# Kernel optimization log

Measured on AMD Instinct MI355X. Metric: run time of the kernel, lower is better.

The kernel has to match this reference:

```python
import jax, jax.numpy as jnp
import numpy as np

N = 50000
E = 800000
H = 8
DH = 32  # hidden 256 / heads 8


def gat_layer(h, src, dst, W, a_src, a_dst, b):
    # h: [N, 256] -> per-head projected features [N, H, DH]
    hp = (h @ W).reshape(N, H, DH)
    # per-node attention logits for src/dst roles: [N, H]
    s_src = jnp.einsum('nhd,hd->nh', hp, a_src)
    s_dst = jnp.einsum('nhd,hd->nh', hp, a_dst)
    e = jax.nn.leaky_relu(s_src[src] + s_dst[dst], negative_slope=0.2)  # [Et, H]
    # segment softmax over incoming edges of each dst node
    m = jax.ops.segment_max(e, dst, num_segments=N)  # [N, H]
    ex = jnp.exp(e - m[dst])
    denom = jax.ops.segment_sum(ex, dst, num_segments=N)  # [N, H] (>0: self-loops)
    alpha = ex / denom[dst]  # [Et, H]
    out = jax.ops.segment_sum(alpha[:, :, None] * hp[src], dst, num_segments=N)
    return out.reshape(N, H * DH) + b


def han_forward(x, edges, proj_W, proj_b, gat_W, gat_asrc, gat_adst, gat_b,
                sem_W1, sem_b1, sem_W2, cls_W1, cls_b1, cls_W2, cls_b2):
    h0 = x @ proj_W + proj_b  # [N, 256]
    loop = jnp.arange(N, dtype=edges.dtype)
    embs = []
    for p in range(edges.shape[0]):  # 3 meta-paths (fixed, small)
        src = jnp.concatenate([edges[p, 0], loop])  # add self-loops (PyG default)
        dst = jnp.concatenate([edges[p, 1], loop])
        h = h0
        for l in range(2):  # 2 GAT layers per meta-path
            h = gat_layer(h, src, dst, gat_W[p, l], gat_asrc[p, l], gat_adst[p, l], gat_b[p, l])
            h = jax.nn.elu(h)  # dropout: eval-mode no-op
        embs.append(h)
    emb = jnp.stack(embs, axis=1)  # [N, P, 256]
    scores = (jnp.tanh(emb @ sem_W1 + sem_b1) @ sem_W2).squeeze(-1)  # [N, P]
    w = jax.nn.softmax(scores, axis=1)
    z = jnp.sum(emb * w[:, :, None], axis=1)  # [N, 256]
    hcls = jax.nn.relu(z @ cls_W1 + cls_b1)
    logits = hcls @ cls_W2 + cls_b2  # [N, 2]
    return logits


def setup_inputs() -> dict:
    key = jax.random.key(0)
    ks = jax.random.split(key, 16)
    s = 0.05
    return {
        'x': jax.random.normal(ks[0], (N, 128), jnp.float32),
        'edges': jax.random.randint(ks[1], (3, 2, E), 0, N, dtype=jnp.int32),
        'proj_W': jax.random.normal(ks[2], (128, 256), jnp.float32) * s,
        'proj_b': jnp.zeros((256,), jnp.float32),
        'gat_W': jax.random.normal(ks[3], (3, 2, 256, 256), jnp.float32) * s,
        'gat_asrc': jax.random.normal(ks[4], (3, 2, H, DH), jnp.float32) * s,
        'gat_adst': jax.random.normal(ks[5], (3, 2, H, DH), jnp.float32) * s,
        'gat_b': jnp.zeros((3, 2, 256), jnp.float32),
        'sem_W1': jax.random.normal(ks[6], (256, 128), jnp.float32) * s,
        'sem_b1': jnp.zeros((128,), jnp.float32),
        'sem_W2': jax.random.normal(ks[7], (128, 1), jnp.float32) * s,
        'cls_W1': jax.random.normal(ks[8], (256, 128), jnp.float32) * s,
        'cls_b1': jnp.zeros((128,), jnp.float32),
        'cls_W2': jax.random.normal(ks[9], (128, 2), jnp.float32) * s,
        'cls_b2': jnp.zeros((2,), jnp.float32),
    }


def reference(x, edges, proj_W, proj_b, gat_W, gat_asrc, gat_adst, gat_b,
              sem_W1, sem_b1, sem_W2, cls_W1, cls_b1, cls_W2, cls_b2):
    return han_forward(x, edges, proj_W, proj_b, gat_W, gat_asrc, gat_adst, gat_b,
                       sem_W1, sem_b1, sem_W2, cls_W1, cls_b1, cls_W2, cls_b2)
```

## Files before the change

kernel.cpp:

```cpp
#include <hip/hip_runtime.h>
#include <hip/hip_fp16.h>
#include <math.h>

#define N_NODES 50000
#define N_EDG   800000
#define NH      8
#define DH      32
#define HID     256
#define MAXD    64

typedef __attribute__((ext_vector_type(8))) short bf16x8;
typedef __attribute__((ext_vector_type(4))) float f32x4;

__device__ __forceinline__ unsigned short f2bf(float x) {
    unsigned u = __float_as_uint(x);
    u += 0x7FFF + ((u >> 16) & 1);
    return (unsigned short)(u >> 16);
}
__device__ __forceinline__ float bf2f(unsigned short h) {
    return __uint_as_float(((unsigned)h) << 16);
}
__device__ __forceinline__ void split8(const float4& a, const float4& b,
                                       uint4& hi, uint4& lo) {
    float v[8] = {a.x,a.y,a.z,a.w,b.x,b.y,b.z,b.w};
    unsigned short h[8], l[8];
    #pragma unroll
    for (int i = 0; i < 8; ++i) { h[i] = f2bf(v[i]); l[i] = f2bf(v[i] - bf2f(h[i])); }
    hi = make_uint4(h[0]|((unsigned)h[1]<<16), h[2]|((unsigned)h[3]<<16),
                    h[4]|((unsigned)h[5]<<16), h[6]|((unsigned)h[7]<<16));
    lo = make_uint4(l[0]|((unsigned)l[1]<<16), l[2]|((unsigned)l[3]<<16),
                    l[4]|((unsigned)l[5]<<16), l[6]|((unsigned)l[7]<<16));
}
__device__ __forceinline__ void h8_to_pair(uint4 r, uint4& hi, uint4& lo) {
    const __half2* hp = (const __half2*)&r;
    unsigned short h[8], l[8];
    #pragma unroll
    for (int i = 0; i < 4; ++i) {
        float2 f = __half22float2(hp[i]);
        h[2*i]   = f2bf(f.x); l[2*i]   = f2bf(f.x - bf2f(h[2*i]));
        h[2*i+1] = f2bf(f.y); l[2*i+1] = f2bf(f.y - bf2f(h[2*i+1]));
    }
    hi = make_uint4(h[0]|((unsigned)h[1]<<16), h[2]|((unsigned)h[3]<<16),
                    h[4]|((unsigned)h[5]<<16), h[6]|((unsigned)h[7]<<16));
    lo = make_uint4(l[0]|((unsigned)l[1]<<16), l[2]|((unsigned)l[3]<<16),
                    l[4]|((unsigned)l[5]<<16), l[6]|((unsigned)l[7]<<16));
}
__device__ __forceinline__ void gll16(const unsigned short* g, unsigned short* l) {
    __builtin_amdgcn_global_load_lds(
        (const __attribute__((address_space(1))) void*)g,
        (__attribute__((address_space(3))) void*)l, 16, 0, 0);
}

template<int NC, int ACT, int OUTMODE, int AMODE>
__global__ __launch_bounds__(256)
void mfma_gemm_k(const float* __restrict__ A32p, const __half* __restrict__ A16p,
                 int lda,
                 const unsigned short* __restrict__ WThi,
                 const unsigned short* __restrict__ WTlo,
                 const float* __restrict__ bias,
                 float* __restrict__ C, __half* __restrict__ Ch,
                 int ldc, int M, int K) {
    __shared__ unsigned short sAh[128*32], sAl[128*32], sBh[128*32], sBl[128*32];
    const int tid  = threadIdx.x;
    const int lane = tid & 63;
    const int w    = tid >> 6;
    const int wr   = w >> 1, wc = w & 1;
    const int r0   = blockIdx.x * 128;
    const int c0   = blockIdx.y * 128;
    const int l15  = lane & 15, q = lane >> 4;

    const int cl8   = (((lane & 3) ^ ((lane >> 4) & 3)) << 3);
    const int lrow  = w*32 + (lane >> 2);
    const int gbrow0 = c0 + lrow, gbrow1 = c0 + lrow + 16;
    const int lbase = w * 1024;

    const int srow = tid >> 2, slot = tid & 3;
    const size_t ga0 = (size_t)min(r0 + srow,      M - 1) * lda + slot * 8;
    const size_t ga1 = (size_t)min(r0 + srow + 64, M - 1) * lda + slot * 8;
    const int lda0 = srow*32 + ((slot ^ ((srow >> 2) & 3)) << 3);
    const int lda1 = lda0 + 64*32;

    f32x4 acc[4][4];
    #pragma unroll
    for (int i = 0; i < 4; ++i)
        #pragma unroll
        for (int j = 0; j < 4; ++j) acc[i][j] = (f32x4){0.f, 0.f, 0.f, 0.f};

    const int swzF = (l15 >> 2) & 3;
    const int qs   = ((q ^ swzF) << 3);

    const int nsteps = K >> 5;
    for (int s = 0; s < nsteps; ++s) {
        const int kc = s << 5;
        __syncthreads();
        uint4 h0, l0, h1, l1;
        if constexpr (AMODE == 0) {
            float4 f0a = *(const float4*)&A32p[ga0 + kc];
            float4 f0b = *(const float4*)&A32p[ga0 + kc + 4];
            float4 f1a = *(const float4*)&A32p[ga1 + kc];
            float4 f1b = *(const float4*)&A32p[ga1 + kc + 4];
            split8(f0a, f0b, h0, l0);
            split8(f1a, f1b, h1, l1);
        } else {
            uint4 r0v = *(const uint4*)&A16p[ga0 + kc];
            uint4 r1v = *(const uint4*)&A16p[ga1 + kc];
            h8_to_pair(r0v, h0, l0);
            h8_to_pair(r1v, h1, l1);
        }
        *(uint4*)&sAh[lda0] = h0; *(uint4*)&sAl[lda0] = l0;
        *(uint4*)&sAh[lda1] = h1; *(uint4*)&sAl[lda1] = l1;
        gll16(&WThi[(size_t)gbrow0*K + kc + cl8], &sBh[lbase]);
        gll16(&WThi[(size_t)gbrow1*K + kc + cl8], &sBh[lbase + 512]);
        gll16(&WTlo[(size_t)gbrow0*K + kc + cl8], &sBl[lbase]);
        gll16(&WTlo[(size_t)gbrow1*K + kc + cl8], &sBl[lbase + 512]);
        __syncthreads();

        bf16x8 fAh[4], fAl[4];
        #pragma unroll
        for (int t = 0; t < 4; ++t) {
            int ra = (wr*64 + t*16 + l15) * 32 + qs;
            fAh[t] = *(const bf16x8*)&sAh[ra];
            fAl[t] = *(const bf16x8*)&sAl[ra];
        }
        #pragma unroll
        for (int nt = 0; nt < 4; ++nt) {
            int rb = (wc*64 + nt*16 + l15) * 32 + qs;
            bf16x8 fBh = *(const bf16x8*)&sBh[rb];
            bf16x8 fBl = *(const bf16x8*)&sBl[rb];
            #pragma unroll
            for (int mt = 0; mt < 4; ++mt) {
                acc[mt][nt] = __builtin_amdgcn_mfma_f32_16x16x32_bf16(fAh[mt], fBh, acc[mt][nt], 0, 0, 0);
                acc[mt][nt] = __builtin_amdgcn_mfma_f32_16x16x32_bf16(fAh[mt], fBl, acc[mt][nt], 0, 0, 0);
                acc[mt][nt] = __builtin_amdgcn_mfma_f32_16x16x32_bf16(fAl[mt], fBh, acc[mt][nt], 0, 0, 0);
            }
        }
    }
    #pragma unroll
    for (int mt = 0; mt < 4; ++mt)
        #pragma unroll
        for (int nt = 0; nt < 4; ++nt) {
            int col = c0 + wc*64 + nt*16 + l15;
            float bb = bias ? bias[col] : 0.f;
            #pragma unroll
            for (int r = 0; r < 4; ++r) {
                int grow = r0 + wr*64 + mt*16 + q*4 + r;
                if (grow < M) {
                    float v = acc[mt][nt][r] + bb;
                    if (ACT == 1) v = tanhf(v);
                    else if (ACT == 2) v = fmaxf(v, 0.f);
                    size_t o = (size_t)grow * ldc + col;
                    if (OUTMODE == 2) Ch[o] = __float2half(v);
                    else              C[o] = v;
                }
            }
        }
}

__global__ __launch_bounds__(256)
void mfma_gemm3_k(const __half* __restrict__ A16p, int aoffz, int lda,
                  const unsigned short* __restrict__ WT, int l,
                  __half* __restrict__ hp3, int M) {
    __shared__ unsigned short sAh[128*32], sAl[128*32], sBh[128*32], sBl[128*32];
    const int p = blockIdx.z;
    A16p += (size_t)p * aoffz;
    const unsigned short* WThi = WT + (size_t)(2*p + l) * 131072;
    const unsigned short* WTlo = WThi + 65536;
    __half* Ch = hp3 + (size_t)p * N_NODES * HID;
    const int K = HID;

    const int tid  = threadIdx.x;
    const int lane = tid & 63;
    const int w    = tid >> 6;
    const int wr   = w >> 1, wc = w & 1;
    const int r0   = blockIdx.x * 128;
    const int c0   = blockIdx.y * 128;
    const int l15  = lane & 15, q = lane >> 4;

    const int cl8   = (((lane & 3) ^ ((lane >> 4) & 3)) << 3);
    const int lrow  = w*32 + (lane >> 2);
    const int gbrow0 = c0 + lrow, gbrow1 = c0 + lrow + 16;
    const int lbase = w * 1024;

    const int srow = tid >> 2, slot = tid & 3;
    const size_t ga0 = (size_t)min(r0 + srow,      M - 1) * lda + slot * 8;
    const size_t ga1 = (size_t)min(r0 + srow + 64, M - 1) * lda + slot * 8;
    const int lda0 = srow*32 + ((slot ^ ((srow >> 2) & 3)) << 3);
    const int lda1 = lda0 + 64*32;

    f32x4 acc[4][4];
    #pragma unroll
    for (int i = 0; i < 4; ++i)
        #pragma unroll
        for (int j = 0; j < 4; ++j) acc[i][j] = (f32x4){0.f, 0.f, 0.f, 0.f};

    const int swzF = (l15 >> 2) & 3;
    const int qs   = ((q ^ swzF) << 3);

    for (int s = 0; s < 8; ++s) {
        const int kc = s << 5;
        __syncthreads();
        uint4 r0v = *(const uint4*)&A16p[ga0 + kc];
        uint4 r1v = *(const uint4*)&A16p[ga1 + kc];
        uint4 h0, l0, h1, l1;
        h8_to_pair(r0v, h0, l0);
        h8_to_pair(r1v, h1, l1);
        *(uint4*)&sAh[lda0] = h0; *(uint4*)&sAl[lda0] = l0;
        *(uint4*)&sAh[lda1] = h1; *(uint4*)&sAl[lda1] = l1;
        gll16(&WThi[(size_t)gbrow0*K + kc + cl8], &sBh[lbase]);
        gll16(&WThi[(size_t)gbrow1*K + kc + cl8], &sBh[lbase + 512]);
        gll16(&WTlo[(size_t)gbrow0*K + kc + cl8], &sBl[lbase]);
        gll16(&WTlo[(size_t)gbrow1*K + kc + cl8], &sBl[lbase + 512]);
        __syncthreads();

        bf16x8 fAh[4], fAl[4];
        #pragma unroll
        for (int t = 0; t < 4; ++t) {
            int ra = (wr*64 + t*16 + l15) * 32 + qs;
            fAh[t] = *(const bf16x8*)&sAh[ra];
            fAl[t] = *(const bf16x8*)&sAl[ra];
        }
        #pragma unroll
        for (int nt = 0; nt < 4; ++nt) {
            int rb = (wc*64 + nt*16 + l15) * 32 + qs;
            bf16x8 fBh = *(const bf16x8*)&sBh[rb];
            bf16x8 fBl = *(const bf16x8*)&sBl[rb];
            #pragma unroll
            for (int mt = 0; mt < 4; ++mt) {
                acc[mt][nt] = __builtin_amdgcn_mfma_f32_16x16x32_bf16(fAh[mt], fBh, acc[mt][nt], 0, 0, 0);
                acc[mt][nt] = __builtin_amdgcn_mfma_f32_16x16x32_bf16(fAh[mt], fBl, acc[mt][nt], 0, 0, 0);
                acc[mt][nt] = __builtin_amdgcn_mfma_f32_16x16x32_bf16(fAl[mt], fBh, acc[mt][nt], 0, 0, 0);
            }
        }
    }
    #pragma unroll
    for (int mt = 0; mt < 4; ++mt)
        #pragma unroll
        for (int nt = 0; nt < 4; ++nt) {
            int col = c0 + wc*64 + nt*16 + l15;
            #pragma unroll
            for (int r = 0; r < 4; ++r) {
                int grow = r0 + wr*64 + mt*16 + q*4 + r;
                if (grow < M)
                    Ch[(size_t)grow * HID + col] = __float2half(acc[mt][nt][r]);
            }
        }
}

__global__ __launch_bounds__(256)
void cvtWall_k(const float* __restrict__ gatW, const float* __restrict__ projW,
               const float* __restrict__ semW1, const float* __restrict__ clsW1,
               unsigned short* __restrict__ WT) {
    int y = blockIdx.y;
    const float* W; int K, N;
    if (y < 6)       { W = gatW + (size_t)y * 65536; K = 256; N = 256; }
    else if (y == 6) { W = projW; K = 128; N = 256; }
    else if (y == 7) { W = semW1; K = 256; N = 128; }
    else             { W = clsW1; K = 256; N = 128; }
    int idx = blockIdx.x * 256 + threadIdx.x;
    if (idx >= K * N) return;
    unsigned short* hi = WT + (size_t)y * 131072;
    unsigned short* lo = hi + 65536;
    int k = idx / N, n = idx - k * N;
    float v = W[idx];
    unsigned short h = f2bf(v);
    hi[n * K + k] = h;
    lo[n * K + k] = f2bf(v - bf2f(h));
}

__global__ __launch_bounds__(256)
void attn_scores3_k(const __half* __restrict__ hp3,
                    const float* __restrict__ gatAs, const float* __restrict__ gatAd,
                    int l, float* __restrict__ ssrc3, float* __restrict__ sdst3) {
    int p = blockIdx.y;
    int gid = blockIdx.x * 256 + threadIdx.x;
    if (gid >= N_NODES * NH) return;
    int h = gid & 7;
    const __half2* hv = (const __half2*)(hp3 + (size_t)p * N_NODES * HID + (size_t)gid * DH);
    const float* a = gatAs + (2*p + l) * HID + h * DH;
    const float* d = gatAd + (2*p + l) * HID + h * DH;
    float ss = 0.f, sd = 0.f;
    #pragma unroll
    for (int j = 0; j < 8; ++j) {
        float4 av = ((const float4*)a)[j], dv = ((const float4*)d)[j];
        float2 f0 = __half22float2(hv[2*j]);
        float2 f1 = __half22float2(hv[2*j + 1]);
        ss += f0.x*av.x + f0.y*av.y + f1.x*av.z + f1.y*av.w;
        sd += f0.x*dv.x + f0.y*dv.y + f1.x*dv.z + f1.y*dv.w;
    }
    ssrc3[p * N_NODES * NH + gid] = ss;
    sdst3[p * N_NODES * NH + gid] = sd;
}

__global__ __launch_bounds__(256)
void zero_k(int* p, int n) { int i = blockIdx.x*256 + threadIdx.x; if (i < n) p[i] = 0; }

__global__ __launch_bounds__(256)
void fill1_k(const int* __restrict__ edges, int* __restrict__ cnt3,
             unsigned short* __restrict__ slots3) {
    int e = blockIdx.x*256 + threadIdx.x;
    if (e >= 3*N_EDG) return;
    int p = e / N_EDG, i = e - p * N_EDG;
    const int* src = edges + (size_t)p * 2 * N_EDG;
    const int* dst = src + N_EDG;
    int s = src[i], d = dst[i];
    s = min(max(s, 0), N_NODES - 1);
    d = min(max(d, 0), N_NODES - 1);
    int pos = atomicAdd(&cnt3[p * N_NODES + d], 1);
    if (pos < MAXD)
        slots3[((size_t)p * N_NODES + d) * MAXD + pos] = (unsigned short)s;
}

__global__ __launch_bounds__(256)
void agg3_k(const int* __restrict__ cnt3, const unsigned short* __restrict__ slots3,
            const float* __restrict__ ssrc3, const float* __restrict__ sdst3,
            const __half* __restrict__ hp3, const float* __restrict__ gatB, int l,
            __half* __restrict__ emb16) {
    const int p = blockIdx.y;
    int wid  = (blockIdx.x * blockDim.x + threadIdx.x) >> 6;
    int lane = threadIdx.x & 63;
    if (wid >= N_NODES) return;
    const int n = wid;
    const unsigned short* srcs = slots3 + ((size_t)p * N_NODES + n) * MAXD;
    const float* s_src = ssrc3 + p * N_NODES * NH;
    const float* s_dst = sdst3 + p * N_NODES * NH;
    const __half* hp = hp3 + (size_t)p * N_NODES * HID;
    const float* bias = gatB + (2*p + l) * HID;
    const int deg = min(cnt3[p * N_NODES + n], MAXD);

    const int sub = lane & 31, eo = lane >> 5;
    const int h2  = sub >> 2;
    const float sd2 = s_dst[n*NH + h2];
    float dn = 0.f;
    float a0=0.f,a1=0.f,a2=0.f,a3=0.f,a4=0.f,a5=0.f,a6=0.f,a7=0.f;
    for (int i = eo; i < deg; i += 2) {
        int s = srcs[i];
        float ev = s_src[s*NH + h2] + sd2;
        ev = ev > 0.f ? ev : 0.2f * ev;
        float ww = __expf(ev);
        dn += ww;
        const __half2* hv = (const __half2*)(hp + (size_t)s * HID + sub * 8);
        __half2 p0 = hv[0], p1 = hv[1], p2 = hv[2], p3 = hv[3];
        float2 f0 = __half22float2(p0), f1 = __half22float2(p1);
        float2 f2 = __half22float2(p2), f3 = __half22float2(p3);
        a0 += ww*f0.x; a1 += ww*f0.y; a2 += ww*f1.x; a3 += ww*f1.y;
        a4 += ww*f2.x; a5 += ww*f2.y; a6 += ww*f3.x; a7 += ww*f3.y;
    }
    dn += __shfl_xor(dn, 32);
    a0 += __shfl_xor(a0, 32); a1 += __shfl_xor(a1, 32);
    a2 += __shfl_xor(a2, 32); a3 += __shfl_xor(a3, 32);
    a4 += __shfl_xor(a4, 32); a5 += __shfl_xor(a5, 32);
    a6 += __shfl_xor(a6, 32); a7 += __shfl_xor(a7, 32);
    if (lane < 32) {
        float evs = s_src[n*NH + h2] + sd2;
        evs = evs > 0.f ? evs : 0.2f * evs;
        float ws = __expf(evs);
        dn += ws;
        const __half2* hv = (const __half2*)(hp + (size_t)n * HID + sub * 8);
        float2 f0 = __half22float2(hv[0]), f1 = __half22float2(hv[1]);
        float2 f2 = __half22float2(hv[2]), f3 = __half22float2(hv[3]);
        a0 += ws*f0.x; a1 += ws*f0.y; a2 += ws*f1.x; a3 += ws*f1.y;
        a4 += ws*f2.x; a5 += ws*f2.y; a6 += ws*f3.x; a7 += ws*f3.y;

        float rdn = 1.f / dn;
        float v[8] = {a0,a1,a2,a3,a4,a5,a6,a7};
        const float4 b0 = *(const float4*)&bias[sub*8];
        const float4 b1 = *(const float4*)&bias[sub*8 + 4];
        v[0]=v[0]*rdn+b0.x; v[1]=v[1]*rdn+b0.y; v[2]=v[2]*rdn+b0.z; v[3]=v[3]*rdn+b0.w;
        v[4]=v[4]*rdn+b1.x; v[5]=v[5]*rdn+b1.y; v[6]=v[6]*rdn+b1.z; v[7]=v[7]*rdn+b1.w;
        unsigned short hh[8];
        #pragma unroll
        for (int k = 0; k < 8; ++k) {
            float e = v[k] > 0.f ? v[k] : expm1f(v[k]);
            hh[k] = __half_as_ushort(__float2half(e));
        }
        size_t o = (size_t)n * 768 + p * HID + sub * 8;
        *(uint4*)&emb16[o] = make_uint4(hh[0]|((unsigned)hh[1]<<16), hh[2]|((unsigned)hh[3]<<16),
                                        hh[4]|((unsigned)hh[5]<<16), hh[6]|((unsigned)hh[7]<<16));
    }
}

__global__ __launch_bounds__(256)
void score_z_k(const float* t, const float* __restrict__ W2,
               const __half* __restrict__ emb16, float* z) {
    int wid  = (blockIdx.x * blockDim.x + threadIdx.x) >> 6;
    int lane = threadIdx.x & 63;
    if (wid >= N_NODES) return;
    const int n = wid;
    float sc[3];
    #pragma unroll
    for (int p = 0; p < 3; ++p) {
        const float* tr = t + (size_t)(n*3 + p) * 128;
        float part = tr[lane] * W2[lane] + tr[64 + lane] * W2[64 + lane];
        #pragma unroll
        for (int o = 1; o < 64; o <<= 1) part += __shfl_xor(part, o);
        sc[p] = part;
    }
    float m  = fmaxf(sc[0], fmaxf(sc[1], sc[2]));
    float e0 = __expf(sc[0]-m), e1 = __expf(sc[1]-m), e2 = __expf(sc[2]-m);
    float rs = 1.f / (e0 + e1 + e2);
    e0 *= rs; e1 *= rs; e2 *= rs;
    const __half* er = emb16 + (size_t)n * 768;
    for (int c = lane; c < 256; c += 64) {
        float v0 = __half2float(er[c]);
        float v1 = __half2float(er[256 + c]);
        float v2 = __half2float(er[512 + c]);
        z[(size_t)n*384 + c] = e0*v0 + e1*v1 + e2*v2;
    }
}

__global__ __launch_bounds__(256)
void logits_k(const float* __restrict__ hcls, const float* __restrict__ W2,
              const float* __restrict__ b2, float* __restrict__ out) {
    int gid = blockIdx.x*256 + threadIdx.x;
    if (gid >= N_NODES * 2) return;
    int n = gid >> 1, o = gid & 1;
    const float* hr = hcls + (size_t)n * 128;
    float a = b2[o];
    #pragma unroll 4
    for (int j = 0; j < 128; ++j) a += hr[j] * W2[j*2 + o];
    out[gid] = a;
}

extern "C" void kernel_launch(void* const* d_in, const int* in_sizes, int n_in,
                              void* d_out, int out_size, void* d_ws, size_t ws_size,
                              hipStream_t stream) {
    (void)in_sizes; (void)n_in; (void)out_size; (void)ws_size;
    const float* x     = (const float*)d_in[0];
    const int*   edges = (const int*)  d_in[1];
    const float* projW = (const float*)d_in[2];
    const float* projb = (const float*)d_in[3];
    const float* gatW  = (const float*)d_in[4];
    const float* gatAs = (const float*)d_in[5];
    const float* gatAd = (const float*)d_in[6];
    const float* gatB  = (const float*)d_in[7];
    const float* semW1 = (const float*)d_in[8];
    const float* semb1 = (const float*)d_in[9];
    const float* semW2 = (const float*)d_in[10];
    const float* clsW1 = (const float*)d_in[11];
    const float* clsb1 = (const float*)d_in[12];
    const float* clsW2 = (const float*)d_in[13];
    const float* clsb2 = (const float*)d_in[14];
    float* out = (float*)d_out;

    char* base = (char*)d_ws;
    const size_t PLANE = (size_t)N_NODES * HID * 2;
    __half* hp3   = (__half*)(base);
    __half* emb16 = (__half*)(base + 3*PLANE);
    __half* h016  = (__half*)(base + 6*PLANE);
    char* small = base + 7*PLANE;
    float* ssrc3 = (float*)small;
    float* sdst3 = ssrc3 + 3*(size_t)N_NODES*NH;
    int*   cnt3  = (int*)(sdst3 + 3*(size_t)N_NODES*NH);
    unsigned short* WT = (unsigned short*)(cnt3 + 3*N_NODES);
    unsigned short* slots3 = WT + 9*131072;
    float* tbuf = (float*)base;
    float* hcls = (float*)(base + 6*PLANE);

    dim3 blk(256);
    const int gx = (N_NODES + 127) / 128;

    cvtWall_k<<<dim3(256, 9), blk, 0, stream>>>(gatW, projW, semW1, clsW1, WT);
    zero_k  <<<(3*N_NODES+255)/256, blk, 0, stream>>>(cnt3, 3*N_NODES);
    fill1_k <<<(3*N_EDG+255)/256,   blk, 0, stream>>>(edges, cnt3, slots3);

    mfma_gemm_k<256,0,2,0><<<dim3(gx,2), blk, 0, stream>>>(
        x, nullptr, 128, WT + 6*131072, WT + 6*131072 + 65536, projb,
        nullptr, h016, 256, N_NODES, 128);

    for (int l = 0; l < 2; ++l) {
        if (l == 0)
            mfma_gemm3_k<<<dim3(gx,2,3), blk, 0, stream>>>(
                h016, 0, HID, WT, 0, hp3, N_NODES);
        else
            mfma_gemm3_k<<<dim3(gx,2,3), blk, 0, stream>>>(
                emb16, HID, 3*HID, WT, 1, hp3, N_NODES);
        attn_scores3_k<<<dim3((N_NODES*NH+255)/256, 3), blk, 0, stream>>>(
            hp3, gatAs, gatAd, l, ssrc3, sdst3);
        agg3_k<<<dim3((N_NODES*64)/256, 3), blk, 0, stream>>>(
            cnt3, slots3, ssrc3, sdst3, hp3, gatB, l, emb16);
    }

    mfma_gemm_k<128,1,0,1><<<dim3((150000+127)/128, 1), blk, 0, stream>>>(
        nullptr, emb16, 256, WT + 7*131072, WT + 7*131072 + 65536, semb1,
        tbuf, nullptr, 128, 150000, 256);
    score_z_k<<<(N_NODES*64)/256, blk, 0, stream>>>(tbuf, semW2, emb16, tbuf);
    mfma_gemm_k<128,2,0,0><<<dim3(gx, 1), blk, 0, stream>>>(
        tbuf, nullptr, 384, WT + 8*131072, WT + 8*131072 + 65536, clsb1,
        hcls, nullptr, 128, N_NODES, 256);
    logits_k<<<(N_NODES*2+255)/256, blk, 0, stream>>>(hcls, clsW2, clsb2, out);
}
```

Before: 1.062 ms.

## Switch split-precision GEMMs from bf16 to scaled fp16 and drop A lo-split

Replaces the bf16 hi/lo split emulation of fp32 GEMMs with an fp16 hi plus scaled fp16 lo split. The lo part is multiplied by 2048 to avoid underflow and accumulated separately. Because the A operand is already fp16, the gemm3 and AMODE 1 paths now load it directly into LDS with global_load_lds. That removes the per-element conversion and split work and one of the three MFMAs per tile. The risks are lower accuracy for the dropped A-lo term and fp16 range limits, plus more registers from the second accumulator set.

After: 1.116 ms. 1.05x slower.

```diff
diff --git a/kernel.cpp b/kernel.cpp
--- a/kernel.cpp
+++ b/kernel.cpp
@@ -8,44 +8,28 @@
 #define DH      32
 #define HID     256
 #define MAXD    64
-
-typedef __attribute__((ext_vector_type(8))) short bf16x8;
+#define LOSC    2048.0f
+#define RLOSC   4.8828125e-4f
+
+typedef __attribute__((ext_vector_type(8))) _Float16 f16x8;
 typedef __attribute__((ext_vector_type(4))) float f32x4;
 
-__device__ __forceinline__ unsigned short f2bf(float x) {
-    unsigned u = __float_as_uint(x);
-    u += 0x7FFF + ((u >> 16) & 1);
-    return (unsigned short)(u >> 16);
-}
-__device__ __forceinline__ float bf2f(unsigned short h) {
-    return __uint_as_float(((unsigned)h) << 16);
-}
-__device__ __forceinline__ void split8(const float4& a, const float4& b,
-                                       uint4& hi, uint4& lo) {
+__device__ __forceinline__ void splitH8(const float4& a, const float4& b,
+                                        uint4& hi, uint4& lo) {
     float v[8] = {a.x,a.y,a.z,a.w,b.x,b.y,b.z,b.w};
     unsigned short h[8], l[8];
     #pragma unroll
-    for (int i = 0; i < 8; ++i) { h[i] = f2bf(v[i]); l[i] = f2bf(v[i] - bf2f(h[i])); }
+    for (int i = 0; i < 8; ++i) {
+        __half hh = __float2half(v[i]);
+        h[i] = __half_as_ushort(hh);
+        l[i] = __half_as_ushort(__float2half((v[i] - __half2float(hh)) * LOSC));
+    }
     hi = make_uint4(h[0]|((unsigned)h[1]<<16), h[2]|((unsigned)h[3]<<16),
                     h[4]|((unsigned)h[5]<<16), h[6]|((unsigned)h[7]<<16));
     lo = make_uint4(l[0]|((unsigned)l[1]<<16), l[2]|((unsigned)l[3]<<16),
                     l[4]|((unsigned)l[5]<<16), l[6]|((unsigned)l[7]<<16));
 }
-__device__ __forceinline__ void h8_to_pair(uint4 r, uint4& hi, uint4& lo) {
-    const __half2* hp = (const __half2*)&r;
-    unsigned short h[8], l[8];
-    #pragma unroll
-    for (int i = 0; i < 4; ++i) {
-        float2 f = __half22float2(hp[i]);
-        h[2*i]   = f2bf(f.x); l[2*i]   = f2bf(f.x - bf2f(h[2*i]));
-        h[2*i+1] = f2bf(f.y); l[2*i+1] = f2bf(f.y - bf2f(h[2*i+1]));
-    }
-    hi = make_uint4(h[0]|((unsigned)h[1]<<16), h[2]|((unsigned)h[3]<<16),
-                    h[4]|((unsigned)h[5]<<16), h[6]|((unsigned)h[7]<<16));
-    lo = make_uint4(l[0]|((unsigned)l[1]<<16), l[2]|((unsigned)l[3]<<16),
-                    l[4]|((unsigned)l[5]<<16), l[6]|((unsigned)l[7]<<16));
-}
-__device__ __forceinline__ void gll16(const unsigned short* g, unsigned short* l) {
+__device__ __forceinline__ void gll16(const void* g, void* l) {
     __builtin_amdgcn_global_load_lds(
         (const __attribute__((address_space(1))) void*)g,
         (__attribute__((address_space(3))) void*)l, 16, 0, 0);
@@ -71,6 +55,8 @@
 
     const int cl8   = (((lane & 3) ^ ((lane >> 4) & 3)) << 3);
     const int lrow  = w*32 + (lane >> 2);
+    const int garow0 = min(r0 + lrow,      M - 1);
+    const int garow1 = min(r0 + lrow + 16, M - 1);
     const int gbrow0 = c0 + lrow, gbrow1 = c0 + lrow + 16;
     const int lbase = w * 1024;
 
@@ -80,11 +66,14 @@
     const int lda0 = srow*32 + ((slot ^ ((srow >> 2) & 3)) << 3);
     const int lda1 = lda0 + 64*32;
 
-    f32x4 acc[4][4];
+    f32x4 acc1[4][4], acc2[4][4];
     #pragma unroll
     for (int i = 0; i < 4; ++i)
         #pragma unroll
-        for (int j = 0; j < 4; ++j) acc[i][j] = (f32x4){0.f, 0.f, 0.f, 0.f};
+        for (int j = 0; j < 4; ++j) {
+            acc1[i][j] = (f32x4){0.f, 0.f, 0.f, 0.f};
+            acc2[i][j] = (f32x4){0.f, 0.f, 0.f, 0.f};
+        }
 
     const int swzF = (l15 >> 2) & 3;
     const int qs   = ((q ^ swzF) << 3);
@@ -93,45 +82,44 @@
     for (int s = 0; s < nsteps; ++s) {
         const int kc = s << 5;
         __syncthreads();
-        uint4 h0, l0, h1, l1;
         if constexpr (AMODE == 0) {
             float4 f0a = *(const float4*)&A32p[ga0 + kc];
             float4 f0b = *(const float4*)&A32p[ga0 + kc + 4];
             float4 f1a = *(const float4*)&A32p[ga1 + kc];
             float4 f1b = *(const float4*)&A32p[ga1 + kc + 4];
-            split8(f0a, f0b, h0, l0);
-            split8(f1a, f1b, h1, l1);
+            uint4 h0, l0, h1, l1;
+            splitH8(f0a, f0b, h0, l0);
+            splitH8(f1a, f1b, h1, l1);
+            *(uint4*)&sAh[lda0] = h0; *(uint4*)&sAl[lda0] = l0;
+            *(uint4*)&sAh[lda1] = h1; *(uint4*)&sAl[lda1] = l1;
         } else {
-            uint4 r0v = *(const uint4*)&A16p[ga0 + kc];
-            uint4 r1v = *(const uint4*)&A16p[ga1 + kc];
-            h8_to_pair(r0v, h0, l0);
-            h8_to_pair(r1v, h1, l1);
-        }
-        *(uint4*)&sAh[lda0] = h0; *(uint4*)&sAl[lda0] = l0;
-        *(uint4*)&sAh[lda1] = h1; *(uint4*)&sAl[lda1] = l1;
+            gll16(&A16p[(size_t)garow0*lda + kc + cl8], &sAh[lbase]);
+            gll16(&A16p[(size_t)garow1*lda + kc + cl8], &sAh[lbase + 512]);
+        }
         gll16(&WThi[(size_t)gbrow0*K + kc + cl8], &sBh[lbase]);
         gll16(&WThi[(size_t)gbrow1*K + kc + cl8], &sBh[lbase + 512]);
         gll16(&WTlo[(size_t)gbrow0*K + kc + cl8], &sBl[lbase]);
         gll16(&WTlo[(size_t)gbrow1*K + kc + cl8], &sBl[lbase + 512]);
         __syncthreads();
 
-        bf16x8 fAh[4], fAl[4];
+        f16x8 fAh[4], fAl[4];
         #pragma unroll
         for (int t = 0; t < 4; ++t) {
             int ra = (wr*64 + t*16 + l15) * 32 + qs;
-            fAh[t] = *(const bf16x8*)&sAh[ra];
-            fAl[t] = *(const bf16x8*)&sAl[ra];
+            fAh[t] = *(const f16x8*)&sAh[ra];
+            if constexpr (AMODE == 0) fAl[t] = *(const f16x8*)&sAl[ra];
         }
         #pragma unroll
         for (int nt = 0; nt < 4; ++nt) {
             int rb = (wc*64 + nt*16 + l15) * 32 + qs;
-            bf16x8 fBh = *(const bf16x8*)&sBh[rb];
-            bf16x8 fBl = *(const bf16x8*)&sBl[rb];
+            f16x8 fBh = *(const f16x8*)&sBh[rb];
+            f16x8 fBl = *(const f16x8*)&sBl[rb];
             #pragma unroll
             for (int mt = 0; mt < 4; ++mt) {
-                acc[mt][nt] = __builtin_amdgcn_mfma_f32_16x16x32_bf16(fAh[mt], fBh, acc[mt][nt], 0, 0, 0);
-                acc[mt][nt] = __builtin_amdgcn_mfma_f32_16x16x32_bf16(fAh[mt], fBl, acc[mt][nt], 0, 0, 0);
-                acc[mt][nt] = __builtin_amdgcn_mfma_f32_16x16x32_bf16(fAl[mt], fBh, acc[mt][nt], 0, 0, 0);
+                acc1[mt][nt] = __builtin_amdgcn_mfma_f32_16x16x32_f16(fAh[mt], fBh, acc1[mt][nt], 0, 0, 0);
+                acc2[mt][nt] = __builtin_amdgcn_mfma_f32_16x16x32_f16(fAh[mt], fBl, acc2[mt][nt], 0, 0, 0);
+                if constexpr (AMODE == 0)
+                    acc2[mt][nt] = __builtin_amdgcn_mfma_f32_16x16x32_f16(fAl[mt], fBh, acc2[mt][nt], 0, 0, 0);
             }
         }
     }
@@ -145,7 +133,7 @@
             for (int r = 0; r < 4; ++r) {
                 int grow = r0 + wr*64 + mt*16 + q*4 + r;
                 if (grow < M) {
-                    float v = acc[mt][nt][r] + bb;
+                    float v = acc1[mt][nt][r] + acc2[mt][nt][r] * RLOSC + bb;
                     if (ACT == 1) v = tanhf(v);
                     else if (ACT == 2) v = fmaxf(v, 0.f);
                     size_t o = (size_t)grow * ldc + col;
@@ -160,7 +148,7 @@
 void mfma_gemm3_k(const __half* __restrict__ A16p, int aoffz, int lda,
                   const unsigned short* __restrict__ WT, int l,
                   __half* __restrict__ hp3, int M) {
-    __shared__ unsigned short sAh[128*32], sAl[128*32], sBh[128*32], sBl[128*32];
+    __shared__ unsigned short sA[128*32], sBh[128*32], sBl[128*32];
     const int p = blockIdx.z;
     A16p += (size_t)p * aoffz;
     const unsigned short* WThi = WT + (size_t)(2*p + l) * 131072;
@@ -178,20 +166,19 @@
 
     const int cl8   = (((lane & 3) ^ ((lane >> 4) & 3)) << 3);
     const int lrow  = w*32 + (lane >> 2);
+    const int garow0 = min(r0 + lrow,      M - 1);
+    const int garow1 = min(r0 + lrow + 16, M - 1);
     const int gbrow0 = c0 + lrow, gbrow1 = c0 + lrow + 16;
     const int lbase = w * 1024;
 
-    const int srow = tid >> 2, slot = tid & 3;
-    const size_t ga0 = (size_t)min(r0 + srow,      M - 1) * lda + slot * 8;
-    const size_t ga1 = (size_t)min(r0 + srow + 64, M - 1) * lda + slot * 8;
-    const int lda0 = srow*32 + ((slot ^ ((srow >> 2) & 3)) << 3);
-    const int lda1 = lda0 + 64*32;
-
-    f32x4 acc[4][4];
+    f32x4 acc1[4][4], acc2[4][4];
     #pragma unroll
     for (int i = 0; i < 4; ++i)
         #pragma unroll
-        for (int j = 0; j < 4; ++j) acc[i][j] = (f32x4){0.f, 0.f, 0.f, 0.f};
+        for (int j = 0; j < 4; ++j) {
+            acc1[i][j] = (f32x4){0.f, 0.f, 0.f, 0.f};
+            acc2[i][j] = (f32x4){0.f, 0.f, 0.f, 0.f};
+        }
 
     const int swzF = (l15 >> 2) & 3;
     const int qs   = ((q ^ swzF) << 3);
@@ -199,36 +186,29 @@
     for (int s = 0; s < 8; ++s) {
         const int kc = s << 5;
         __syncthreads();
-        uint4 r0v = *(const uint4*)&A16p[ga0 + kc];
-        uint4 r1v = *(const uint4*)&A16p[ga1 + kc];
-        uint4 h0, l0, h1, l1;
-        h8_to_pair(r0v, h0, l0);
-        h8_to_pair(r1v, h1, l1);
-        *(uint4*)&sAh[lda0] = h0; *(uint4*)&sAl[lda0] = l0;
-        *(uint4*)&sAh[lda1] = h1; *(uint4*)&sAl[lda1] = l1;
+        gll16(&A16p[(size_t)garow0*lda + kc + cl8], &sA[lbase]);
+        gll16(&A16p[(size_t)garow1*lda + kc + cl8], &sA[lbase + 512]);
         gll16(&WThi[(size_t)gbrow0*K + kc + cl8], &sBh[lbase]);
         gll16(&WThi[(size_t)gbrow1*K + kc + cl8], &sBh[lbase + 512]);
         gll16(&WTlo[(size_t)gbrow0*K + kc + cl8], &sBl[lbase]);
         gll16(&WTlo[(size_t)gbrow1*K + kc + cl8], &sBl[lbase + 512]);
         __syncthreads();
 
-        bf16x8 fAh[4], fAl[4];
+        f16x8 fA[4];
         #pragma unroll
         for (int t = 0; t < 4; ++t) {
             int ra = (wr*64 + t*16 + l15) * 32 + qs;
-            fAh[t] = *(const bf16x8*)&sAh[ra];
-            fAl[t] = *(const bf16x8*)&sAl[ra];
+            fA[t] = *(const f16x8*)&sA[ra];
         }
         #pragma unroll
         for (int nt = 0; nt < 4; ++nt) {
             int rb = (wc*64 + nt*16 + l15) * 32 + qs;
-            bf16x8 fBh = *(const bf16x8*)&sBh[rb];
-            bf16x8 fBl = *(const bf16x8*)&sBl[rb];
+            f16x8 fBh = *(const f16x8*)&sBh[rb];
+            f16x8 fBl = *(const f16x8*)&sBl[rb];
             #pragma unroll
             for (int mt = 0; mt < 4; ++mt) {
-                acc[mt][nt] = __builtin_amdgcn_mfma_f32_16x16x32_bf16(fAh[mt], fBh, acc[mt][nt], 0, 0, 0);
-                acc[mt][nt] = __builtin_amdgcn_mfma_f32_16x16x32_bf16(fAh[mt], fBl, acc[mt][nt], 0, 0, 0);
-                acc[mt][nt] = __builtin_amdgcn_mfma_f32_16x16x32_bf16(fAl[mt], fBh, acc[mt][nt], 0, 0, 0);
+                acc1[mt][nt] = __builtin_amdgcn_mfma_f32_16x16x32_f16(fA[mt], fBh, acc1[mt][nt], 0, 0, 0);
+                acc2[mt][nt] = __builtin_amdgcn_mfma_f32_16x16x32_f16(fA[mt], fBl, acc2[mt][nt], 0, 0, 0);
             }
         }
     }
@@ -241,7 +221,8 @@
             for (int r = 0; r < 4; ++r) {
                 int grow = r0 + wr*64 + mt*16 + q*4 + r;
                 if (grow < M)
-                    Ch[(size_t)grow * HID + col] = __float2half(acc[mt][nt][r]);
+                    Ch[(size_t)grow * HID + col] =
+                        __float2half(acc1[mt][nt][r] + acc2[mt][nt][r] * RLOSC);
             }
         }
 }
@@ -262,9 +243,9 @@
     unsigned short* lo = hi + 65536;
     int k = idx / N, n = idx - k * N;
     float v = W[idx];
-    unsigned short h = f2bf(v);
-    hi[n * K + k] = h;
-    lo[n * K + k] = f2bf(v - bf2f(h));
+    __half h = __float2half(v);
+    hi[n * K + k] = __half_as_ushort(h);
+    lo[n * K + k] = __half_as_ushort(__float2half((v - __half2float(h)) * LOSC));
 }
 
 __global__ __launch_bounds__(256)
```
